# Kernel tuning notes

Measured on AMD Instinct MI355X. Metric: run time of the kernel, lower is better.

The kernel has to match this reference:

```python
import jax, jax.numpy as jnp
import numpy as np

N, E, G = 64, 128, 4
D0, ED = 9, 4
H1, H2, H3 = 2000, 500, 100
F1, F2, F3 = 1000, 100, 50


def setup_inputs() -> dict:
    key = jax.random.key(0)
    ks = iter(jax.random.split(key, 32))

    def p(shape, s=0.02):
        return (jax.random.normal(next(ks), shape, jnp.float32) * s)

    inp = {
        "x": jax.random.normal(next(ks), (N, D0), jnp.float32),
        "edge_index": jax.random.randint(next(ks), (2, E), 0, N),
        "edge_attr": jax.random.normal(next(ks), (E, ED), jnp.float32),
        "batch": jnp.sort(jax.random.randint(next(ks), (N,), 0, G)),
        # NNConv layer 1: edge MLP Linear(ED, D0*H1), root weight, bias
        "We1": p((ED, D0 * H1)), "be1": p((D0 * H1,)),
        "root1": p((D0, H1)), "b1": p((H1,)),
        # NNConv layer 2
        "We2": p((ED, H1 * H2)), "be2": p((H1 * H2,)),
        "root2": p((H1, H2)), "b2": p((H2,)),
        # NNConv layer 3
        "We3": p((ED, H2 * H3)), "be3": p((H2 * H3,)),
        "root3": p((H2, H3)), "b3": p((H3,)),
        # FCN head
        "W1": p((H3, F1)), "c1": p((F1,)),
        "W2": p((F1, F2)), "c2": p((F2,)),
        "W3": p((F2, F3)), "c3": p((F3,)),
        "W4": p((F3, 1)), "c4": p((1,)),
    }
    return inp


def _nnconv(x, src, dst, edge_attr, We, be, root, b):
    # edge-conditioned weights: [E, in, out]
    in_dim = x.shape[1]
    w = (edge_attr @ We + be).reshape(edge_attr.shape[0], in_dim, -1)
    # gather source feats, per-edge matmul, scatter-add to targets
    msg = jnp.einsum('ei,eio->eo', x[src], w)
    agg = jax.ops.segment_sum(msg, dst, num_segments=x.shape[0])
    return agg + x @ root + b


def reference(x, edge_index, edge_attr, batch,
              We1, be1, root1, b1,
              We2, be2, root2, b2,
              We3, be3, root3, b3,
              W1, c1, W2, c2, W3, c3, W4, c4):
    src, dst = edge_index[0], edge_index[1]
    h = jax.nn.relu(_nnconv(x, src, dst, edge_attr, We1, be1, root1, b1))
    h = jax.nn.relu(_nnconv(h, src, dst, edge_attr, We2, be2, root2, b2))
    h = jax.nn.relu(_nnconv(h, src, dst, edge_attr, We3, be3, root3, b3))
    # sum readout per graph (dropout layers are identity in eval mode)
    g = jax.ops.segment_sum(h, batch, num_segments=G)  # [G, H3]
    g = jax.nn.relu(g @ W1 + c1)
    g = jax.nn.relu(g @ W2 + c2)
    g = jax.nn.relu(g @ W3 + c3)
    out = g @ W4 + c4
    return out.reshape(-1)  # [G]
```

## Files before the change

### kernel.cpp

```cpp
#include <hip/hip_runtime.h>

#define NN 64
#define EE 128
#define GG 4
#define D0 9
#define EDIM 4
#define H1 2000
#define H2 500
#define H3 100
#define FF1 1000
#define FF2 100
#define FF3 50
#define KDIM 384

#define OFF_A    0
#define OFF_Y    24576
#define OFF_PRE1 28032
#define OFF_PRE2 156032
#define OFF_PRE3 188032
#define OFF_N2   194432
#define OFF_N3   386432
#define OFF_F1   424832
#define OFF_F2   428832

#define FILLN 269200

__device__ __forceinline__ void gl2lds16(const float* g, float* l) {
    __builtin_amdgcn_global_load_lds(
        (const __attribute__((address_space(1))) unsigned int*)g,
        (__attribute__((address_space(3))) unsigned int*)l,
        16, 0, 0);
}

__device__ __forceinline__ float4 ldf4(const float* p) {
    return *(const float4*)p;
}

__global__ __launch_bounds__(256) void k_init(
    const float* __restrict__ x, const int* __restrict__ edge_index,
    const float* __restrict__ edge_attr,
    const float* __restrict__ b2, const float* __restrict__ b3,
    const float* __restrict__ c2, float* __restrict__ ws)
{
    const int b = blockIdx.x, tid = threadIdx.x;
    if (b == 0) {
        float* A = ws + OFF_A;
        for (int i = tid; i < NN * KDIM; i += 256) A[i] = 0.f;
        __syncthreads();
        if (tid < EE) {
            int s = edge_index[tid];
            int t = edge_index[EE + tid];
            float* row = A + t * KDIM + s * 6;
            #pragma unroll
            for (int d = 0; d < 4; ++d) atomicAdd(row + d, edge_attr[tid * 4 + d]);
            atomicAdd(row + 4, 1.0f);
        }
        if (tid < NN) A[tid * KDIM + tid * 6 + 5] = 1.0f;
    } else if (b == 1) {
        __shared__ float Ys[NN * 54];
        for (int i = tid; i < NN * 54; i += 256) Ys[i] = 0.f;
        __syncthreads();
        if (tid < EE) {
            int s = edge_index[tid];
            int t = edge_index[EE + tid];
            float ea[4];
            #pragma unroll
            for (int d = 0; d < 4; ++d) ea[d] = edge_attr[tid * 4 + d];
            #pragma unroll
            for (int i = 0; i < D0; ++i) {
                float xv = x[s * D0 + i];
                #pragma unroll
                for (int d = 0; d < 4; ++d)
                    atomicAdd(&Ys[t * 54 + d * 9 + i], ea[d] * xv);
                atomicAdd(&Ys[t * 54 + 36 + i], xv);
            }
        }
        if (tid < NN) {
            #pragma unroll
            for (int i = 0; i < D0; ++i) Ys[tid * 54 + 45 + i] = x[tid * D0 + i];
        }
        __syncthreads();
        for (int i = tid; i < NN * 54; i += 256) ws[OFF_Y + i] = Ys[i];
    } else {
        const int stride = (gridDim.x - 2) * 256;
        for (int i = (b - 2) * 256 + tid; i < FILLN; i += stride) {
            if (i < 32000)         ws[OFF_PRE2 + i] = b2[i % H2];
            else if (i < 38400)  { int j = i - 32000;  ws[OFF_PRE3 + j] = b3[j % H3]; }
            else if (i < 230400)   ws[OFF_N2 + (i - 38400)] = 0.f;
            else if (i < 268800)   ws[OFF_N3 + (i - 230400)] = 0.f;
            else                 { int j = i - 268800; ws[OFF_F2 + j] = c2[j % FF2]; }
        }
    }
}

__global__ __launch_bounds__(256) void k_lin1(
    const float* __restrict__ Yw,
    const float* __restrict__ We1, const float* __restrict__ be1,
    const float* __restrict__ root1, const float* __restrict__ b1,
    float* __restrict__ pre1)
{
    const int tid = threadIdx.x;
    const int tx = tid & 15, ty = tid >> 4;
    const int o0 = blockIdx.x * 64;
    const int w = min(64, H1 - o0);

    __shared__ float Ys[64 * 56];
    __shared__ __align__(16) float Bs[54 * 64];

    for (int i = tid; i < 64 * 54; i += 256) {
        int u = i / 54, r = i - u * 54;
        Ys[u * 56 + r] = Yw[i];
    }
    for (int i = tid; i < 54 * 64; i += 256) {
        int r = i >> 6, c = i & 63;
        int d = r / 9, ii = r - d * 9;
        const float* rowp = ((d < 4) ? (We1 + d * (D0 * H1))
                                     : ((d == 4) ? be1 : root1)) + ii * H1;
        Bs[r * 64 + c] = (c < w) ? rowp[o0 + c] : 0.f;
    }
    __syncthreads();

    float acc[4][4] = {};
    #pragma unroll 6
    for (int r = 0; r < 54; ++r) {
        float a0 = Ys[(ty * 4 + 0) * 56 + r];
        float a1 = Ys[(ty * 4 + 1) * 56 + r];
        float a2 = Ys[(ty * 4 + 2) * 56 + r];
        float a3 = Ys[(ty * 4 + 3) * 56 + r];
        const float4 bv = *(const float4*)&Bs[r * 64 + tx * 4];
        acc[0][0] += a0 * bv.x; acc[0][1] += a0 * bv.y; acc[0][2] += a0 * bv.z; acc[0][3] += a0 * bv.w;
        acc[1][0] += a1 * bv.x; acc[1][1] += a1 * bv.y; acc[1][2] += a1 * bv.z; acc[1][3] += a1 * bv.w;
        acc[2][0] += a2 * bv.x; acc[2][1] += a2 * bv.y; acc[2][2] += a2 * bv.z; acc[2][3] += a2 * bv.w;
        acc[3][0] += a3 * bv.x; acc[3][1] += a3 * bv.y; acc[3][2] += a3 * bv.z; acc[3][3] += a3 * bv.w;
    }
    #pragma unroll
    for (int i = 0; i < 4; ++i) {
        int u = ty * 4 + i;
        #pragma unroll
        for (int jj = 0; jj < 4; ++jj) {
            int j = o0 + tx * 4 + jj;
            if (j < H1) {
                float v = b1[j] + acc[i][jj];
                pre1[u * H1 + j] = v > 0.f ? v : 0.f;
            }
        }
    }
}

template<int KC, int ITERS, bool RELUA>
__global__ __launch_bounds__(256) void k_msg2(
    const float* __restrict__ pre, int K,
    const float* __restrict__ We, const float* __restrict__ be,
    const float* __restrict__ root, long long secSize,
    int M, int OT, int S, float* __restrict__ n)
{
    constexpr int NCH = (64 * KC) / 256;
    const int b  = blockIdx.x;
    const int s  = b % S;
    const int t2 = b / S;
    const int ot = t2 % OT;
    const int d  = t2 / OT;
    const int tid = threadIdx.x;
    const int tx = tid & 15, ty = tid >> 4;
    const int wv = tid >> 6, ln = tid & 63;
    const int o0 = ot * 64;
    const int w  = min(64, M - o0);
    const int kbase = s * (KC * ITERS);

    const float* Bbase = (d < 4) ? (We + (long long)d * secSize)
                                 : ((d == 4) ? be : root);

    __shared__ __align__(16) float As[2][64 * KC];
    __shared__ __align__(16) float Bs[2][KC * 64];

    auto stage = [&](int bf, int kb) {
        for (int c = wv; c < NCH; c += 4) {
            int f = c * 256 + ln * 4;
            int r = f / KC, cc = f - r * KC;
            gl2lds16(pre + r * K + kb + cc, &As[bf][c * 256]);
        }
        for (int c = wv; c < NCH; c += 4) {
            int f = c * 256 + ln * 4;
            int r = f >> 6, col = f & 63;
            if (col < w)
                gl2lds16(Bbase + (long long)(kb + r) * M + o0 + col,
                         &Bs[bf][c * 256]);
        }
    };

    float acc[4][4] = {};
    stage(0, kbase);
    __syncthreads();

    for (int it = 0; it < ITERS; ++it) {
        if (it + 1 < ITERS) stage((it + 1) & 1, kbase + (it + 1) * KC);
        const float* Ab = As[it & 1];
        const float* Bb = Bs[it & 1];
        #pragma unroll
        for (int k4 = 0; k4 < KC / 4; ++k4) {
            float4 av[4], bv[4];
            #pragma unroll
            for (int i = 0; i < 4; ++i)
                av[i] = ldf4(&Ab[(ty * 4 + i) * KC + k4 * 4]);
            #pragma unroll
            for (int q = 0; q < 4; ++q)
                bv[q] = ldf4(&Bb[(k4 * 4 + q) * 64 + tx * 4]);
            if (RELUA) {
                #pragma unroll
                for (int i = 0; i < 4; ++i) {
                    av[i].x = fmaxf(av[i].x, 0.f);
                    av[i].y = fmaxf(av[i].y, 0.f);
                    av[i].z = fmaxf(av[i].z, 0.f);
                    av[i].w = fmaxf(av[i].w, 0.f);
                }
            }
            #pragma unroll
            for (int i = 0; i < 4; ++i) {
                acc[i][0] += av[i].x * bv[0].x; acc[i][1] += av[i].x * bv[0].y;
                acc[i][2] += av[i].x * bv[0].z; acc[i][3] += av[i].x * bv[0].w;
                acc[i][0] += av[i].y * bv[1].x; acc[i][1] += av[i].y * bv[1].y;
                acc[i][2] += av[i].y * bv[1].z; acc[i][3] += av[i].y * bv[1].w;
                acc[i][0] += av[i].z * bv[2].x; acc[i][1] += av[i].z * bv[2].y;
                acc[i][2] += av[i].z * bv[2].z; acc[i][3] += av[i].z * bv[2].w;
                acc[i][0] += av[i].w * bv[3].x; acc[i][1] += av[i].w * bv[3].y;
                acc[i][2] += av[i].w * bv[3].z; acc[i][3] += av[i].w * bv[3].w;
            }
        }
        __syncthreads();
    }

    #pragma unroll
    for (int i = 0; i < 4; ++i) {
        int u = ty * 4 + i;
        #pragma unroll
        for (int jj = 0; jj < 4; ++jj) {
            int j = o0 + tx * 4 + jj;
            if (j < M) atomicAdd(&n[(u * 6 + d) * M + j], acc[i][jj]);
        }
    }
}

__global__ __launch_bounds__(256) void k_agg(
    const float* __restrict__ A, const float* __restrict__ B,
    int M, float* __restrict__ out)
{
    constexpr int KC = 48;
    constexpr int NCH = (64 * KC) / 256;
    const int s  = blockIdx.x & 7;
    const int ot = blockIdx.x >> 3;
    const int tid = threadIdx.x;
    const int tx = tid & 15, ty = tid >> 4;
    const int wv = tid >> 6, ln = tid & 63;
    const int o0 = ot * 64;
    const int w  = min(64, M - o0);
    const int kb = s * KC;

    __shared__ __align__(16) float As[64 * KC];
    __shared__ __align__(16) float Bs[KC * 64];

    for (int c = wv; c < NCH; c += 4) {
        int f = c * 256 + ln * 4;
        int r = f / KC, cc = f - r * KC;
        gl2lds16(A + r * KDIM + kb + cc, &As[c * 256]);
    }
    for (int c = wv; c < NCH; c += 4) {
        int f = c * 256 + ln * 4;
        int r = f >> 6, col = f & 63;
        if (col < w)
            gl2lds16(B + (kb + r) * M + o0 + col, &Bs[c * 256]);
    }
    __syncthreads();

    float acc[4][4] = {};
    #pragma unroll
    for (int k4 = 0; k4 < KC / 4; ++k4) {
        float4 av[4], bv[4];
        #pragma unroll
        for (int i = 0; i < 4; ++i)
            av[i] = ldf4(&As[(ty * 4 + i) * KC + k4 * 4]);
        #pragma unroll
        for (int q = 0; q < 4; ++q)
            bv[q] = ldf4(&Bs[(k4 * 4 + q) * 64 + tx * 4]);
        #pragma unroll
        for (int i = 0; i < 4; ++i) {
            acc[i][0] += av[i].x * bv[0].x; acc[i][1] += av[i].x * bv[0].y;
            acc[i][2] += av[i].x * bv[0].z; acc[i][3] += av[i].x * bv[0].w;
            acc[i][0] += av[i].y * bv[1].x; acc[i][1] += av[i].y * bv[1].y;
            acc[i][2] += av[i].y * bv[1].z; acc[i][3] += av[i].y * bv[1].w;
            acc[i][0] += av[i].z * bv[2].x; acc[i][1] += av[i].z * bv[2].y;
            acc[i][2] += av[i].z * bv[2].z; acc[i][3] += av[i].z * bv[2].w;
            acc[i][0] += av[i].w * bv[3].x; acc[i][1] += av[i].w * bv[3].y;
            acc[i][2] += av[i].w * bv[3].z; acc[i][3] += av[i].w * bv[3].w;
        }
    }
    #pragma unroll
    for (int i = 0; i < 4; ++i) {
        int u = ty * 4 + i;
        #pragma unroll
        for (int jj = 0; jj < 4; ++jj) {
            int j = o0 + tx * 4 + jj;
            if (j < M) atomicAdd(&out[u * M + j], acc[i][jj]);
        }
    }
}

__global__ __launch_bounds__(256) void k_head1(
    const float* __restrict__ pre3, const int* __restrict__ batch,
    const float* __restrict__ W1, const float* __restrict__ c1,
    float* __restrict__ f1)
{
    const int gi = blockIdx.x >> 4;
    const int jt = blockIdx.x & 15;
    const int o0 = jt * 64;
    const int tid = threadIdx.x;
    __shared__ int   bsh[NN];
    __shared__ float gs[H3];
    __shared__ float red[4 * 64];

    if (tid < NN) bsh[tid] = batch[tid];
    __syncthreads();
    for (int d = tid; d < H3; d += 256) {
        float acc = 0.f;
        #pragma unroll
        for (int v = 0; v < NN; ++v) {
            float h = pre3[v * H3 + d];
            h = h > 0.f ? h : 0.f;
            acc += (bsh[v] == gi) ? h : 0.f;
        }
        gs[d] = acc;
    }
    __syncthreads();
    const int jj = tid & 63, kq = tid >> 6;
    const int oc = min(o0 + jj, FF1 - 1);
    float p = 0.f;
    #pragma unroll
    for (int k = kq * 25; k < kq * 25 + 25; ++k)
        p += gs[k] * W1[k * FF1 + oc];
    red[kq * 64 + jj] = p;
    __syncthreads();
    if (tid < 64) {
        int o = o0 + tid;
        if (o < FF1) {
            float v = c1[o] + red[tid] + red[64 + tid] + red[128 + tid] + red[192 + tid];
            f1[gi * FF1 + o] = v > 0.f ? v : 0.f;
        }
    }
}

__global__ __launch_bounds__(256) void k_head2(
    const float* __restrict__ f1, const float* __restrict__ W2,
    float* __restrict__ f2)
{
    const int s = blockIdx.x;
    const int k0 = s * 63;
    const int kn = min(63, FF1 - k0);
    const int tid = threadIdx.x;
    __shared__ float f1s[4 * 63];
    for (int i = tid; i < 4 * kn; i += 256) {
        int gi = i / kn, kk = i - gi * kn;
        f1s[gi * 63 + kk] = f1[gi * FF1 + k0 + kk];
    }
    __syncthreads();
    for (int idx = tid; idx < GG * FF2; idx += 256) {
        int gi = idx / FF2, o = idx - gi * FF2;
        float acc = 0.f;
        for (int kk = 0; kk < kn; ++kk)
            acc += f1s[gi * 63 + kk] * W2[(k0 + kk) * FF2 + o];
        atomicAdd(&f2[idx], acc);
    }
}

__global__ __launch_bounds__(256) void k_head3(
    const float* __restrict__ f2, const float* __restrict__ W3,
    const float* __restrict__ c3, const float* __restrict__ W4,
    const float* __restrict__ c4, float* __restrict__ out)
{
    const int tid = threadIdx.x;
    __shared__ float f2s[GG * FF2];
    __shared__ float f3s[GG * FF3];
    for (int i = tid; i < GG * FF2; i += 256) {
        float v = f2[i];
        f2s[i] = v > 0.f ? v : 0.f;
    }
    __syncthreads();
    if (tid < GG * FF3) {
        int gi = tid / FF3, o = tid - gi * FF3;
        float acc = c3[o];
        for (int k = 0; k < FF2; ++k)
            acc += f2s[gi * FF2 + k] * W3[k * FF3 + o];
        f3s[tid] = acc > 0.f ? acc : 0.f;
    }
    __syncthreads();
    if (tid < GG) {
        float acc = c4[0];
        #pragma unroll
        for (int k = 0; k < FF3; ++k) acc += f3s[tid * FF3 + k] * W4[k];
        out[tid] = acc;
    }
}

extern "C" void kernel_launch(void* const* d_in, const int* in_sizes, int n_in,
                              void* d_out, int out_size, void* d_ws, size_t ws_size,
                              hipStream_t stream) {
    const float* x          = (const float*)d_in[0];
    const int*   edge_index = (const int*)  d_in[1];
    const float* edge_attr  = (const float*)d_in[2];
    const int*   batch      = (const int*)  d_in[3];
    const float* We1 = (const float*)d_in[4];
    const float* be1 = (const float*)d_in[5];
    const float* root1 = (const float*)d_in[6];
    const float* b1  = (const float*)d_in[7];
    const float* We2 = (const float*)d_in[8];
    const float* be2 = (const float*)d_in[9];
    const float* root2 = (const float*)d_in[10];
    const float* b2  = (const float*)d_in[11];
    const float* We3 = (const float*)d_in[12];
    const float* be3 = (const float*)d_in[13];
    const float* root3 = (const float*)d_in[14];
    const float* b3  = (const float*)d_in[15];
    const float* W1 = (const float*)d_in[16];
    const float* c1 = (const float*)d_in[17];
    const float* W2 = (const float*)d_in[18];
    const float* c2 = (const float*)d_in[19];
    const float* W3 = (const float*)d_in[20];
    const float* c3 = (const float*)d_in[21];
    const float* W4 = (const float*)d_in[22];
    const float* c4 = (const float*)d_in[23];
    float* ws  = (float*)d_ws;
    float* out = (float*)d_out;

    k_init<<<66, 256, 0, stream>>>(x, edge_index, edge_attr, b2, b3, c2, ws);
    k_lin1<<<32, 256, 0, stream>>>(ws + OFF_Y, We1, be1, root1, b1, ws + OFF_PRE1);
    k_msg2<20, 10, false><<<480, 256, 0, stream>>>(ws + OFF_PRE1, H1, We2, be2,
                                                   root2, (long long)H1 * H2,
                                                   H2, 8, 10, ws + OFF_N2);
    k_agg<<<64, 256, 0, stream>>>(ws + OFF_A, ws + OFF_N2, H2, ws + OFF_PRE2);
    k_msg2<20, 1, true><<<300, 256, 0, stream>>>(ws + OFF_PRE2, H2, We3, be3,
                                                 root3, (long long)H2 * H3,
                                                 H3, 2, 25, ws + OFF_N3);
    k_agg<<<16, 256, 0, stream>>>(ws + OFF_A, ws + OFF_N3, H3, ws + OFF_PRE3);
    k_head1<<<64, 256, 0, stream>>>(ws + OFF_PRE3, batch, W1, c1, ws + OFF_F1);
    k_head2<<<16, 256, 0, stream>>>(ws + OFF_F1, W2, ws + OFF_F2);
    k_head3<<<1, 256, 0, stream>>>(ws + OFF_F2, W3, c3, W4, c4, out);
}
```

Measured before the change: 248.6 us.

## Aggregate over edges before weight GEMM and use split-K partials instead of atomics

Reorders the NNConv computation for layers 2 and 3. The adjacency-weighted features (Q = A_d · P for each edge-attribute channel, the count and root channels) are formed first, and a single GEMM then runs over the concatenated K dimension against We/be/root. Split-K partial results are written to a buffer and summed by dedicated reduction kernels that add the bias and ReLU, replacing atomicAdd accumulation and the large zero-fill init. The intent is to drop the intermediate per-node 6x message buffer and the separate aggregation GEMM. In exchange it adds extra kernels and a large partial buffer that must be written and read back.

```diff
diff --git a/kernel.cpp b/kernel.cpp
--- a/kernel.cpp
+++ b/kernel.cpp
@@ -11,19 +11,16 @@
 #define FF1 1000
 #define FF2 100
 #define FF3 50
-#define KDIM 384
-
-#define OFF_A    0
+
+#define OFF_ACH  0
 #define OFF_Y    24576
-#define OFF_PRE1 28032
-#define OFF_PRE2 156032
-#define OFF_PRE3 188032
-#define OFF_N2   194432
-#define OFF_N3   386432
-#define OFF_F1   424832
-#define OFF_F2   428832
-
-#define FILLN 269200
+#define OFF_P1   28032
+#define OFF_Q    156032
+#define OFF_PART 924032
+#define OFF_P2   2524032
+#define OFF_PRE3 2556032
+#define OFF_F1   2562432
+#define OFF_F2   2566432
 
 __device__ __forceinline__ void gl2lds16(const float* g, float* l) {
     __builtin_amdgcn_global_load_lds(
@@ -38,24 +35,23 @@
 
 __global__ __launch_bounds__(256) void k_init(
     const float* __restrict__ x, const int* __restrict__ edge_index,
-    const float* __restrict__ edge_attr,
-    const float* __restrict__ b2, const float* __restrict__ b3,
-    const float* __restrict__ c2, float* __restrict__ ws)
+    const float* __restrict__ edge_attr, const float* __restrict__ c2,
+    float* __restrict__ ws)
 {
     const int b = blockIdx.x, tid = threadIdx.x;
     if (b == 0) {
-        float* A = ws + OFF_A;
-        for (int i = tid; i < NN * KDIM; i += 256) A[i] = 0.f;
+        float* A = ws + OFF_ACH;
+        for (int i = tid; i < 6 * NN * NN; i += 256) A[i] = 0.f;
         __syncthreads();
         if (tid < EE) {
             int s = edge_index[tid];
             int t = edge_index[EE + tid];
-            float* row = A + t * KDIM + s * 6;
             #pragma unroll
-            for (int d = 0; d < 4; ++d) atomicAdd(row + d, edge_attr[tid * 4 + d]);
-            atomicAdd(row + 4, 1.0f);
-        }
-        if (tid < NN) A[tid * KDIM + tid * 6 + 5] = 1.0f;
+            for (int d = 0; d < 4; ++d)
+                atomicAdd(A + d * 4096 + t * 64 + s, edge_attr[tid * 4 + d]);
+            atomicAdd(A + 4 * 4096 + t * 64 + s, 1.0f);
+        }
+        if (tid < NN) A[5 * 4096 + tid * 64 + tid] = 1.0f;
     } else if (b == 1) {
         __shared__ float Ys[NN * 54];
         for (int i = tid; i < NN * 54; i += 256) Ys[i] = 0.f;
@@ -82,14 +78,7 @@
         __syncthreads();
         for (int i = tid; i < NN * 54; i += 256) ws[OFF_Y + i] = Ys[i];
     } else {
-        const int stride = (gridDim.x - 2) * 256;
-        for (int i = (b - 2) * 256 + tid; i < FILLN; i += stride) {
-            if (i < 32000)         ws[OFF_PRE2 + i] = b2[i % H2];
-            else if (i < 38400)  { int j = i - 32000;  ws[OFF_PRE3 + j] = b3[j % H3]; }
-            else if (i < 230400)   ws[OFF_N2 + (i - 38400)] = 0.f;
-            else if (i < 268800)   ws[OFF_N3 + (i - 230400)] = 0.f;
-            else                 { int j = i - 268800; ws[OFF_F2 + j] = c2[j % FF2]; }
-        }
+        for (int i = tid; i < GG * FF2; i += 256) ws[OFF_F2 + i] = c2[i % FF2];
     }
 }
 
@@ -147,48 +136,87 @@
     }
 }
 
-template<int KC, int ITERS, bool RELUA>
-__global__ __launch_bounds__(256) void k_msg2(
-    const float* __restrict__ pre, int K,
-    const float* __restrict__ We, const float* __restrict__ be,
-    const float* __restrict__ root, long long secSize,
-    int M, int OT, int S, float* __restrict__ n)
-{
-    constexpr int NCH = (64 * KC) / 256;
-    const int b  = blockIdx.x;
-    const int s  = b % S;
-    const int t2 = b / S;
-    const int ot = t2 % OT;
-    const int d  = t2 / OT;
-    const int tid = threadIdx.x;
-    const int tx = tid & 15, ty = tid >> 4;
+template<int Kd, int KTOT, int NKT>
+__global__ __launch_bounds__(256) void k_q(
+    const float* __restrict__ Ach, const float* __restrict__ P,
+    float* __restrict__ Qf)
+{
+    const int bx = blockIdx.x;
+    const int d = bx / NKT, kt = bx % NKT;
+    const int k0 = kt * 128;
+    const int tid = threadIdx.x;
+    const int kk = tid & 127;
+    const int k = k0 + kk;
+    const int vh = __builtin_amdgcn_readfirstlane(tid >> 7);
+    const int nf4 = min(128, Kd - k0) >> 2;
+
+    __shared__ __align__(16) float Pl[64 * 128];
+    for (int i4 = tid; i4 < 64 * 32; i4 += 256) {
+        int u = i4 >> 5, c4 = i4 & 31;
+        if (c4 < nf4)
+            *(float4*)&Pl[u * 128 + c4 * 4] = ldf4(P + u * Kd + k0 + c4 * 4);
+    }
+    __syncthreads();
+
+    const float* Ad = Ach + d * 4096 + vh * (32 * 64);
+    float acc[32] = {};
+    #pragma unroll 4
+    for (int u4 = 0; u4 < 16; ++u4) {
+        float p0 = Pl[(u4 * 4 + 0) * 128 + kk];
+        float p1 = Pl[(u4 * 4 + 1) * 128 + kk];
+        float p2 = Pl[(u4 * 4 + 2) * 128 + kk];
+        float p3 = Pl[(u4 * 4 + 3) * 128 + kk];
+        #pragma unroll
+        for (int r = 0; r < 32; ++r) {
+            float4 a = ldf4(Ad + r * 64 + u4 * 4);
+            acc[r] += a.x * p0 + a.y * p1 + a.z * p2 + a.w * p3;
+        }
+    }
+    if (k < Kd) {
+        #pragma unroll
+        for (int r = 0; r < 32; ++r)
+            Qf[(vh * 32 + r) * KTOT + d * Kd + k] = acc[r];
+    }
+}
+
+template<int M, int OT, int S, int ITERS, int T1, int T2>
+__global__ __launch_bounds__(256) void k_split(
+    const float* __restrict__ Qf, const float* __restrict__ We,
+    const float* __restrict__ be, const float* __restrict__ root,
+    float* __restrict__ part)
+{
+    constexpr int KC = 20, BN = 32;
+    constexpr int KTOT = S * ITERS * KC;
+    const int b = blockIdx.x;
+    const int s = b % S, ot = b / S;
+    const int o0 = ot * BN;
+    const int tid = threadIdx.x;
+    const int tx = tid & 7, ty = tid >> 3;
     const int wv = tid >> 6, ln = tid & 63;
-    const int o0 = ot * 64;
-    const int w  = min(64, M - o0);
     const int kbase = s * (KC * ITERS);
 
-    const float* Bbase = (d < 4) ? (We + (long long)d * secSize)
-                                 : ((d == 4) ? be : root);
-
     __shared__ __align__(16) float As[2][64 * KC];
-    __shared__ __align__(16) float Bs[2][KC * 64];
+    __shared__ __align__(16) float Bs[2][KC * BN];
 
     auto stage = [&](int bf, int kb) {
-        for (int c = wv; c < NCH; c += 4) {
+        for (int c = wv; c < 5; c += 4) {
             int f = c * 256 + ln * 4;
-            int r = f / KC, cc = f - r * KC;
-            gl2lds16(pre + r * K + kb + cc, &As[bf][c * 256]);
-        }
-        for (int c = wv; c < NCH; c += 4) {
+            int r = f / KC, kkk = f - r * KC;
+            gl2lds16(Qf + r * KTOT + kb + kkk, &As[bf][c * 256]);
+        }
+        for (int c = wv; c < 3; c += 4) {
             int f = c * 256 + ln * 4;
-            int r = f >> 6, col = f & 63;
-            if (col < w)
-                gl2lds16(Bbase + (long long)(kb + r) * M + o0 + col,
-                         &Bs[bf][c * 256]);
+            int krow = (f >> 5) & 31, col = f & 31;
+            int kg = kb + krow;
+            const float* bp = (kg < T1) ? (We + (long long)kg * M)
+                            : (kg < T2) ? (be + (long long)(kg - T1) * M)
+                                        : (root + (long long)(kg - T2) * M);
+            if (f < KC * BN && (o0 + col) < M)
+                gl2lds16(bp + o0 + col, &Bs[bf][c * 256]);
         }
     };
 
-    float acc[4][4] = {};
+    float acc[2][4] = {};
     stage(0, kbase);
     __syncthreads();
 
@@ -198,110 +226,68 @@
         const float* Bb = Bs[it & 1];
         #pragma unroll
         for (int k4 = 0; k4 < KC / 4; ++k4) {
-            float4 av[4], bv[4];
-            #pragma unroll
-            for (int i = 0; i < 4; ++i)
-                av[i] = ldf4(&Ab[(ty * 4 + i) * KC + k4 * 4]);
-            #pragma unroll
-            for (int q = 0; q < 4; ++q)
-                bv[q] = ldf4(&Bb[(k4 * 4 + q) * 64 + tx * 4]);
-            if (RELUA) {
-                #pragma unroll
-                for (int i = 0; i < 4; ++i) {
-                    av[i].x = fmaxf(av[i].x, 0.f);
-                    av[i].y = fmaxf(av[i].y, 0.f);
-                    av[i].z = fmaxf(av[i].z, 0.f);
-                    av[i].w = fmaxf(av[i].w, 0.f);
-                }
-            }
-            #pragma unroll
-            for (int i = 0; i < 4; ++i) {
-                acc[i][0] += av[i].x * bv[0].x; acc[i][1] += av[i].x * bv[0].y;
-                acc[i][2] += av[i].x * bv[0].z; acc[i][3] += av[i].x * bv[0].w;
-                acc[i][0] += av[i].y * bv[1].x; acc[i][1] += av[i].y * bv[1].y;
-                acc[i][2] += av[i].y * bv[1].z; acc[i][3] += av[i].y * bv[1].w;
-                acc[i][0] += av[i].z * bv[2].x; acc[i][1] += av[i].z * bv[2].y;
-                acc[i][2] += av[i].z * bv[2].z; acc[i][3] += av[i].z * bv[2].w;
-                acc[i][0] += av[i].w * bv[3].x; acc[i][1] += av[i].w * bv[3].y;
-                acc[i][2] += av[i].w * bv[3].z; acc[i][3] += av[i].w * bv[3].w;
-            }
+            float4 a0 = ldf4(&Ab[(ty * 2 + 0) * KC + k4 * 4]);
+            float4 a1 = ldf4(&Ab[(ty * 2 + 1) * KC + k4 * 4]);
+            float4 b0 = ldf4(&Bb[(k4 * 4 + 0) * BN + tx * 4]);
+            float4 b1 = ldf4(&Bb[(k4 * 4 + 1) * BN + tx * 4]);
+            float4 b2 = ldf4(&Bb[(k4 * 4 + 2) * BN + tx * 4]);
+            float4 b3 = ldf4(&Bb[(k4 * 4 + 3) * BN + tx * 4]);
+            acc[0][0] += a0.x * b0.x; acc[0][1] += a0.x * b0.y; acc[0][2] += a0.x * b0.z; acc[0][3] += a0.x * b0.w;
+            acc[0][0] += a0.y * b1.x; acc[0][1] += a0.y * b1.y; acc[0][2] += a0.y * b1.z; acc[0][3] += a0.y * b1.w;
+            acc[0][0] += a0.z * b2.x; acc[0][1] += a0.z * b2.y; acc[0][2] += a0.z * b2.z; acc[0][3] += a0.z * b2.w;
+            acc[0][0] += a0.w * b3.x; acc[0][1] += a0.w * b3.y; acc[0][2] += a0.w * b3.z; acc[0][3] += a0.w * b3.w;
+            acc[1][0] += a1.x * b0.x; acc[1][1] += a1.x * b0.y; acc[1][2] += a1.x * b0.z; acc[1][3] += a1.x * b0.w;
+            acc[1][0] += a1.y * b1.x; acc[1][1] += a1.y * b1.y; acc[1][2] += a1.y * b1.z; acc[1][3] += a1.y * b1.w;
+            acc[1][0] += a1.z * b2.x; acc[1][1] += a1.z * b2.y; acc[1][2] += a1.z * b2.z; acc[1][3] += a1.z * b2.w;
+            acc[1][0] += a1.w * b3.x; acc[1][1] += a1.w * b3.y; acc[1][2] += a1.w * b3.z; acc[1][3] += a1.w * b3.w;
         }
         __syncthreads();
     }
 
+    float* dst = part + s * (64 * M);
     #pragma unroll
-    for (int i = 0; i < 4; ++i) {
-        int u = ty * 4 + i;
+    for (int i = 0; i < 2; ++i) {
+        int u = ty * 2 + i;
         #pragma unroll
         for (int jj = 0; jj < 4; ++jj) {
             int j = o0 + tx * 4 + jj;
-            if (j < M) atomicAdd(&n[(u * 6 + d) * M + j], acc[i][jj]);
-        }
-    }
-}
-
-__global__ __launch_bounds__(256) void k_agg(
-    const float* __restrict__ A, const float* __restrict__ B,
-    int M, float* __restrict__ out)
-{
-    constexpr int KC = 48;
-    constexpr int NCH = (64 * KC) / 256;
-    const int s  = blockIdx.x & 7;
-    const int ot = blockIdx.x >> 3;
-    const int tid = threadIdx.x;
-    const int tx = tid & 15, ty = tid >> 4;
-    const int wv = tid >> 6, ln = tid & 63;
-    const int o0 = ot * 64;
-    const int w  = min(64, M - o0);
-    const int kb = s * KC;
-
-    __shared__ __align__(16) float As[64 * KC];
-    __shared__ __align__(16) float Bs[KC * 64];
-
-    for (int c = wv; c < NCH; c += 4) {
-        int f = c * 256 + ln * 4;
-        int r = f / KC, cc = f - r * KC;
-        gl2lds16(A + r * KDIM + kb + cc, &As[c * 256]);
-    }
-    for (int c = wv; c < NCH; c += 4) {
-        int f = c * 256 + ln * 4;
-        int r = f >> 6, col = f & 63;
-        if (col < w)
-            gl2lds16(B + (kb + r) * M + o0 + col, &Bs[c * 256]);
-    }
-    __syncthreads();
-
-    float acc[4][4] = {};
-    #pragma unroll
-    for (int k4 = 0; k4 < KC / 4; ++k4) {
-        float4 av[4], bv[4];
-        #pragma unroll
-        for (int i = 0; i < 4; ++i)
-            av[i] = ldf4(&As[(ty * 4 + i) * KC + k4 * 4]);
-        #pragma unroll
-        for (int q = 0; q < 4; ++q)
-            bv[q] = ldf4(&Bs[(k4 * 4 + q) * 64 + tx * 4]);
-        #pragma unroll
-        for (int i = 0; i < 4; ++i) {
-            acc[i][0] += av[i].x * bv[0].x; acc[i][1] += av[i].x * bv[0].y;
-            acc[i][2] += av[i].x * bv[0].z; acc[i][3] += av[i].x * bv[0].w;
-            acc[i][0] += av[i].y * bv[1].x; acc[i][1] += av[i].y * bv[1].y;
-            acc[i][2] += av[i].y * bv[1].z; acc[i][3] += av[i].y * bv[1].w;
-            acc[i][0] += av[i].z * bv[2].x; acc[i][1] += av[i].z * bv[2].y;
-            acc[i][2] += av[i].z * bv[2].z; acc[i][3] += av[i].z * bv[2].w;
-            acc[i][0] += av[i].w * bv[3].x; acc[i][1] += av[i].w * bv[3].y;
-            acc[i][2] += av[i].w * bv[3].z; acc[i][3] += av[i].w * bv[3].w;
-        }
-    }
-    #pragma unroll
-    for (int i = 0; i < 4; ++i) {
-        int u = ty * 4 + i;
-        #pragma unroll
-        for (int jj = 0; jj < 4; ++jj) {
-            int j = o0 + tx * 4 + jj;
-            if (j < M) atomicAdd(&out[u * M + j], acc[i][jj]);
-        }
-    }
+            if (j < M) dst[u * M + j] = acc[i][jj];
+        }
+    }
+}
+
+__global__ __launch_bounds__(256) void k_red2(
+    const float* __restrict__ part, const float* __restrict__ b2,
+    float* __restrict__ P2)
+{
+    int i4 = blockIdx.x * 256 + threadIdx.x;
+    if (i4 >= (64 * 500) / 4) return;
+    int o = (i4 * 4) % 500;
+    float4 acc = ldf4(b2 + o);
+    #pragma unroll 10
+    for (int s = 0; s < 50; ++s) {
+        float4 v = ldf4(part + s * 32000 + i4 * 4);
+        acc.x += v.x; acc.y += v.y; acc.z += v.z; acc.w += v.w;
+    }
+    acc.x = fmaxf(acc.x, 0.f); acc.y = fmaxf(acc.y, 0.f);
+    acc.z = fmaxf(acc.z, 0.f); acc.w = fmaxf(acc.w, 0.f);
+    *(float4*)(P2 + i4 * 4) = acc;
+}
+
+__global__ __launch_bounds__(256) void k_red3(
+    const float* __restrict__ part, const float* __restrict__ b3,
+    float* __restrict__ pre3)
+{
+    int i4 = blockIdx.x * 256 + threadIdx.x;
+    if (i4 >= (64 * 100) / 4) return;
+    int o = (i4 * 4) % 100;
+    float4 acc = ldf4(b3 + o);
+    #pragma unroll 10
+    for (int s = 0; s < 50; ++s) {
+        float4 v = ldf4(part + s * 6400 + i4 * 4);
+        acc.x += v.x; acc.y += v.y; acc.z += v.z; acc.w += v.w;
+    }
+    *(float4*)(pre3 + i4 * 4) = acc;
 }
 
 __global__ __launch_bounds__(256) void k_head1(
@@ -429,16 +415,18 @@
     float* ws  = (float*)d_ws;
     float* out = (float*)d_out;
 
-    k_init<<<66, 256, 0, stream>>>(x, edge_index, edge_attr, b2, b3, c2, ws);
-    k_lin1<<<32, 256, 0, stream>>>(ws + OFF_Y, We1, be1, root1, b1, ws + OFF_PRE1);
-    k_msg2<20, 10, false><<<480, 256, 0, stream>>>(ws + OFF_PRE1, H1, We2, be2,
-                                                   root2, (long long)H1 * H2,
-                                                   H2, 8, 10, ws + OFF_N2);
-    k_agg<<<64, 256, 0, stream>>>(ws + OFF_A, ws + OFF_N2, H2, ws + OFF_PRE2);
-    k_msg2<20, 1, true><<<300, 256, 0, stream>>>(ws + OFF_PRE2, H2, We3, be3,
-                                                 root3, (long long)H2 * H3,
-                                                 H3, 2, 25, ws + OFF_N3);
-    k_agg<<<16, 256, 0, stream>>>(ws + OFF_A, ws + OFF_N3, H3, ws + OFF_PRE3);
+    k_init<<<3, 256, 0, stream>>>(x, edge_index, edge_attr, c2, ws);
+    k_lin1<<<32, 256, 0, stream>>>(ws + OFF_Y, We1, be1, root1, b1, ws + OFF_P1);
+    k_q<2000, 12000, 16><<<96, 256, 0, stream>>>(ws + OFF_ACH, ws + OFF_P1,
+                                                 ws + OFF_Q);
+    k_split<500, 16, 50, 12, 8000, 10000><<<800, 256, 0, stream>>>(
+        ws + OFF_Q, We2, be2, root2, ws + OFF_PART);
+    k_red2<<<32, 256, 0, stream>>>(ws + OFF_PART, b2, ws + OFF_P2);
+    k_q<500, 3000, 4><<<24, 256, 0, stream>>>(ws + OFF_ACH, ws + OFF_P2,
+                                              ws + OFF_Q);
+    k_split<100, 4, 50, 3, 2000, 2500><<<200, 256, 0, stream>>>(
+        ws + OFF_Q, We3, be3, root3, ws + OFF_PART);
+    k_red3<<<7, 256, 0, stream>>>(ws + OFF_PART, b3, ws + OFF_PRE3);
     k_head1<<<64, 256, 0, stream>>>(ws + OFF_PRE3, batch, W1, c1, ws + OFF_F1);
     k_head2<<<16, 256, 0, stream>>>(ws + OFF_F1, W2, ws + OFF_F2);
     k_head3<<<1, 256, 0, stream>>>(ws + OFF_F2, W3, c3, W4, c4, out);
```

Result: slower. 332.8 us (+33.9%).
